# Kernel tuning notes

Measured on AMD Instinct MI355X. Metric: run time of the kernel, lower is better.

The kernel has to match this reference:

```python
import jax, jax.numpy as jnp
import numpy as np

N = 100_000
E = 1_000_000
D = 64
NORM_FACTOR = 100.0
LN_EPS = 1e-5


def setup_inputs() -> dict:
    key = jax.random.key(0)
    ks = jax.random.split(key, 8)
    h = jax.random.normal(ks[0], (N, D), dtype=jnp.float32)
    distances = jax.random.uniform(ks[1], (E, 1), dtype=jnp.float32)
    edges = jax.random.randint(ks[2], (2, E), 0, N, dtype=jnp.int64)
    node_mask = jnp.ones((N, 1), dtype=jnp.float32)
    edge_mask = jnp.ones((E, 1), dtype=jnp.float32)
    s = 1.0 / np.sqrt(D)
    W_lin = jax.random.normal(ks[3], (D, D), dtype=jnp.float32) * s
    b_lin = jnp.zeros((D,), dtype=jnp.float32)
    att_W1 = jax.random.normal(ks[4], (D, 2 * D + 1), dtype=jnp.float32) * (1.0 / np.sqrt(2 * D + 1))
    att_b1 = jnp.zeros((D,), dtype=jnp.float32)
    att_W2 = jax.random.normal(ks[5], (1, D), dtype=jnp.float32) * s
    att_b2 = jnp.zeros((1,), dtype=jnp.float32)
    ln_g = jnp.ones((D,), dtype=jnp.float32)
    ln_b = jnp.zeros((D,), dtype=jnp.float32)
    return {"h": h, "distances": distances, "edges": edges, "node_mask": node_mask,
            "edge_mask": edge_mask, "W_lin": W_lin, "b_lin": b_lin,
            "att_W1": att_W1, "att_b1": att_b1, "att_W2": att_W2, "att_b2": att_b2,
            "ln_g": ln_g, "ln_b": ln_b}


def reference(h, distances, edges, node_mask, edge_mask, W_lin, b_lin,
              att_W1, att_b1, att_W2, att_b2, ln_g, ln_b):
    # Linear projection: [N, D]
    x = h @ W_lin.T + b_lin
    row, col = edges[0], edges[1]
    x_row = x[row]          # [E, D]
    x_col = x[col]          # [E, D]
    # DenseAtt: MLP(concat(x_row, x_col, dist)) -> sigmoid -> * edge_mask
    cat = jnp.concatenate([x_row, x_col, distances], axis=1)  # [E, 2D+1]
    hdn = jax.nn.silu(cat @ att_W1.T + att_b1)                # [E, D]
    att = jax.nn.sigmoid(hdn @ att_W2.T + att_b2) * edge_mask # [E, 1]
    # Attention-weighted scatter-sum aggregation into row segments
    agg = x_col * att
    out = jax.ops.segment_sum(agg, row, num_segments=x.shape[0]) / NORM_FACTOR
    out = out + x           # residual
    # LayerNorm + activation
    mu = jnp.mean(out, axis=-1, keepdims=True)
    var = jnp.mean(jnp.square(out - mu), axis=-1, keepdims=True)
    y = (out - mu) * jax.lax.rsqrt(var + LN_EPS) * ln_g + ln_b
    return jax.nn.silu(y)
```

## Files before the change

kernel.cpp:

```cpp
#include <hip/hip_runtime.h>
#include <hip/hip_bf16.h>

#define N_NODES 100000
#define N_EDGES 1000000
#define DIM 64
#define NORM_INV 0.01f
#define LN_EPS 1e-5f
#define N_TILES 6250
#define PROJ_BLOCKS 1563
#define N_BUCKETS 782
#define NB_PAD 800
#define HISTB 489
#define SC_EDGES 4096
#define SC_BLOCKS 245
#define L2E 1.4426950408889634f
#define LN2 0.6931471805599453f
#define CAP 2560

typedef __attribute__((ext_vector_type(8))) short short8;
typedef __attribute__((ext_vector_type(4))) float f32x4;

__device__ __forceinline__ unsigned short f2bf(float f) {
    union { float f; unsigned u; } x; x.f = f;
    unsigned r = x.u + 0x7FFFu + ((x.u >> 16) & 1u);
    return (unsigned short)(r >> 16);
}
__device__ __forceinline__ float bf2f(unsigned short s) {
    union { unsigned u; float f; } x; x.u = ((unsigned)s) << 16; return x.f;
}

__global__ __launch_bounds__(256) void prep_frags(
    const float* __restrict__ W, const float* __restrict__ att_W1,
    const float* __restrict__ att_b1, const float* __restrict__ att_W2,
    short8* __restrict__ whi, short8* __restrict__ wlo,
    short8* __restrict__ wa, short8* __restrict__ wb,
    float4* __restrict__ tab) {
    const int l = threadIdx.x & 63;
    const int nt = threadIdx.x >> 6;
    const int c = l & 15, q = l >> 4;
    const int n = nt * 16 + c;
#pragma unroll
    for (int ks = 0; ks < 2; ++ks) {
        const int k0 = ks * 32 + q * 8;
        short8 hi8, lo8, a8, b8;
#pragma unroll
        for (int jj = 0; jj < 8; ++jj) {
            float w = W[n * 64 + k0 + jj];
            unsigned short hh = f2bf(w);
            hi8[jj] = (short)hh;
            lo8[jj] = (short)f2bf(w - bf2f(hh));
            a8[jj] = (short)f2bf(att_W1[n * 129 + k0 + jj]);
            b8[jj] = (short)f2bf(att_W1[n * 129 + 64 + k0 + jj]);
        }
        const int idx = (nt * 2 + ks) * 64 + l;
        whi[idx] = hi8; wlo[idx] = lo8; wa[idx] = a8; wb[idx] = b8;
    }
    if (threadIdx.x < 64) {
        const int f = threadIdx.x;
        tab[f] = make_float4(att_W2[f] * LN2, att_W1[f * 129 + 128] * L2E,
                             att_b1[f] * L2E, 0.f);
    }
}

__global__ __launch_bounds__(256) void proj_hist(
    const float* __restrict__ h, const float* __restrict__ bl,
    const short8* __restrict__ whi, const short8* __restrict__ wlo,
    const short8* __restrict__ wa, const short8* __restrict__ wb,
    const int* __restrict__ edges, int* __restrict__ bucketCnt,
    unsigned short* __restrict__ xv, unsigned short* __restrict__ u_bf) {
    if (blockIdx.x >= PROJ_BLOCKS) {
        __shared__ int lh[N_BUCKETS];
        const int tid = threadIdx.x;
        for (int i = tid; i < N_BUCKETS; i += 256) lh[i] = 0;
        __syncthreads();
        const int e0 = (blockIdx.x - PROJ_BLOCKS) * 2048;
#pragma unroll
        for (int i = 0; i < 8; ++i) {
            const int e = e0 + tid * 8 + i;
            if (e < N_EDGES) atomicAdd(&lh[edges[e] >> 7], 1);
        }
        __syncthreads();
        for (int b = tid; b < N_BUCKETS; b += 256)
            if (lh[b]) atomicAdd(&bucketCnt[b], lh[b]);
        return;
    }
    __shared__ __align__(16) unsigned short lds[4][16 * 72];
    const int lane = threadIdx.x & 63;
    const int wv = threadIdx.x >> 6;
    const int c = lane & 15, q = lane >> 4;
    const int tile = blockIdx.x * 4 + wv;
    if (tile >= N_TILES) return;
    const int n0 = tile * 16;

    short8 Whi[4][2], Wlo[4][2], Wa[4][2], Wb[4][2];
    float bias[4];
#pragma unroll
    for (int nt = 0; nt < 4; ++nt) {
        bias[nt] = bl[nt * 16 + c];
#pragma unroll
        for (int ks = 0; ks < 2; ++ks) {
            const int idx = (nt * 2 + ks) * 64 + lane;
            Whi[nt][ks] = whi[idx]; Wlo[nt][ks] = wlo[idx];
            Wa[nt][ks] = wa[idx];   Wb[nt][ks] = wb[idx];
        }
    }

    short8 Ahi[2], Alo[2];
#pragma unroll
    for (int ks = 0; ks < 2; ++ks) {
        const float* hp = h + (size_t)(n0 + c) * 64 + ks * 32 + q * 8;
        f32x4 p0 = *(const f32x4*)hp;
        f32x4 p1 = *(const f32x4*)(hp + 4);
        short8 hi8, lo8;
#pragma unroll
        for (int jj = 0; jj < 4; ++jj) {
            unsigned short hh = f2bf(p0[jj]);
            hi8[jj] = (short)hh; lo8[jj] = (short)f2bf(p0[jj] - bf2f(hh));
            unsigned short h2 = f2bf(p1[jj]);
            hi8[4 + jj] = (short)h2; lo8[4 + jj] = (short)f2bf(p1[jj] - bf2f(h2));
        }
        Ahi[ks] = hi8; Alo[ks] = lo8;
    }

    f32x4 xacc[4] = {{0,0,0,0},{0,0,0,0},{0,0,0,0},{0,0,0,0}};
#pragma unroll
    for (int ks = 0; ks < 2; ++ks)
#pragma unroll
        for (int nt = 0; nt < 4; ++nt) {
            xacc[nt] = __builtin_amdgcn_mfma_f32_16x16x32_bf16(Ahi[ks], Whi[nt][ks], xacc[nt], 0, 0, 0);
            xacc[nt] = __builtin_amdgcn_mfma_f32_16x16x32_bf16(Ahi[ks], Wlo[nt][ks], xacc[nt], 0, 0, 0);
            xacc[nt] = __builtin_amdgcn_mfma_f32_16x16x32_bf16(Alo[ks], Whi[nt][ks], xacc[nt], 0, 0, 0);
        }

    unsigned short* lw = lds[wv];
#pragma unroll
    for (int r = 0; r < 4; ++r) {
        const int node = n0 + q * 4 + r;
        unsigned short xb[4];
#pragma unroll
        for (int nt = 0; nt < 4; ++nt) {
            unsigned short v16 = f2bf(xacc[nt][r] + bias[nt]);
            xb[nt] = v16;
            lw[(q * 4 + r) * 72 + nt * 16 + c] = v16;
        }
        uint2 pk;
        pk.x = (unsigned)xb[0] | ((unsigned)xb[1] << 16);
        pk.y = (unsigned)xb[2] | ((unsigned)xb[3] << 16);
        *(uint2*)(xv + (size_t)node * 128 + c * 8) = pk;
    }

    short8 Ax[2];
#pragma unroll
    for (int ks = 0; ks < 2; ++ks)
        Ax[ks] = *(const short8*)&lw[c * 72 + ks * 32 + q * 8];

    f32x4 uacc[4] = {{0,0,0,0},{0,0,0,0},{0,0,0,0},{0,0,0,0}};
    f32x4 vacc[4] = {{0,0,0,0},{0,0,0,0},{0,0,0,0},{0,0,0,0}};
#pragma unroll
    for (int ks = 0; ks < 2; ++ks)
#pragma unroll
        for (int nt = 0; nt < 4; ++nt) {
            uacc[nt] = __builtin_amdgcn_mfma_f32_16x16x32_bf16(Ax[ks], Wa[nt][ks], uacc[nt], 0, 0, 0);
            vacc[nt] = __builtin_amdgcn_mfma_f32_16x16x32_bf16(Ax[ks], Wb[nt][ks], vacc[nt], 0, 0, 0);
        }
#pragma unroll
    for (int r = 0; r < 4; ++r) {
        const int node = n0 + q * 4 + r;
        uint2 pu;
        pu.x = (unsigned)f2bf(uacc[0][r] * L2E) | ((unsigned)f2bf(uacc[1][r] * L2E) << 16);
        pu.y = (unsigned)f2bf(uacc[2][r] * L2E) | ((unsigned)f2bf(uacc[3][r] * L2E) << 16);
        *(uint2*)(u_bf + (size_t)node * 64 + c * 4) = pu;
        uint2 pk;
        pk.x = (unsigned)f2bf(vacc[0][r] * L2E) | ((unsigned)f2bf(vacc[1][r] * L2E) << 16);
        pk.y = (unsigned)f2bf(vacc[2][r] * L2E) | ((unsigned)f2bf(vacc[3][r] * L2E) << 16);
        *(uint2*)(xv + (size_t)node * 128 + c * 8 + 4) = pk;
    }
}

__global__ __launch_bounds__(1024) void scanA(
    const int* __restrict__ bucketCnt, int* __restrict__ baseA,
    int* __restrict__ cursA) {
    __shared__ int wsum[16];
    const int t = threadIdx.x, lane = t & 63, w = t >> 6;
    const int v = (t < N_BUCKETS) ? bucketCnt[t] : 0;
    int sc = v;
#pragma unroll
    for (int off = 1; off < 64; off <<= 1) {
        int u = __shfl_up(sc, off);
        if (lane >= off) sc += u;
    }
    if (lane == 63) wsum[w] = sc;
    __syncthreads();
    if (w == 0) {
        int x = (lane < 16) ? wsum[lane] : 0;
#pragma unroll
        for (int off = 1; off < 16; off <<= 1) {
            int u = __shfl_up(x, off);
            if (lane >= off) x += u;
        }
        if (lane < 16) wsum[lane] = x;
    }
    __syncthreads();
    const int excl = sc - v + ((w > 0) ? wsum[w - 1] : 0);
    if (t < N_BUCKETS) { baseA[t] = excl; cursA[t] = excl; }
    if (t == N_BUCKETS - 1) baseA[N_BUCKETS] = excl + v;
}

__global__ __launch_bounds__(256) void scatterB(
    const int* __restrict__ edges, const float* __restrict__ dist,
    const float* __restrict__ emask, int* __restrict__ cursA,
    uint2* __restrict__ srec) {
    __shared__ int lh[NB_PAD];
    __shared__ int lofs[NB_PAD];
    __shared__ int lb[NB_PAD];
    __shared__ __align__(16) uint2 lsort[SC_EDGES];
    __shared__ unsigned short gb[SC_EDGES];
    __shared__ int wsum[4];

    const int tid = threadIdx.x;
    const int lane = tid & 63;
    const int w = tid >> 6;
    for (int i = tid; i < NB_PAD; i += 256) lh[i] = 0;
    __syncthreads();

    const int eb = blockIdx.x * SC_EDGES;
    const int total = min(SC_EDGES, N_EDGES - eb);

    int rows[16], rank[16];
    uint2 recs[16];
    const int e0 = eb + tid * 16;
#pragma unroll
    for (int g = 0; g < 4; ++g) {
        const int e = e0 + g * 4;
        if (e + 4 <= N_EDGES) {
            const int4 rr = *(const int4*)(edges + e);
            const int4 cc = *(const int4*)(edges + N_EDGES + e);
            const float4 dd = *(const float4*)(dist + e);
            const float4 mm = *(const float4*)(emask + e);
            rows[g*4+0] = rr.x; rows[g*4+1] = rr.y; rows[g*4+2] = rr.z; rows[g*4+3] = rr.w;
            const int c4[4] = {cc.x, cc.y, cc.z, cc.w};
            const float d4[4] = {dd.x, dd.y, dd.z, dd.w};
            const float m4[4] = {mm.x, mm.y, mm.z, mm.w};
#pragma unroll
            for (int i = 0; i < 4; ++i) {
                const int ii = g * 4 + i;
                recs[ii].x = (unsigned)c4[i] | ((unsigned)(rows[ii] & 127) << 24);
                recs[ii].y = (unsigned)f2bf(d4[i]) |
                             ((unsigned)f2bf(m4[i] * NORM_INV) << 16);
                rank[ii] = atomicAdd(&lh[rows[ii] >> 7], 1);
            }
        } else {
#pragma unroll
            for (int i = 0; i < 4; ++i) {
                const int ii = g * 4 + i;
                const int ee = e + i;
                if (ee < N_EDGES) {
                    rows[ii] = edges[ee];
                    recs[ii].x = (unsigned)edges[N_EDGES + ee] |
                                 ((unsigned)(rows[ii] & 127) << 24);
                    recs[ii].y = (unsigned)f2bf(dist[ee]) |
                                 ((unsigned)f2bf(emask[ee] * NORM_INV) << 16);
                    rank[ii] = atomicAdd(&lh[rows[ii] >> 7], 1);
                } else {
                    rows[ii] = -1;
                }
            }
        }
    }
    __syncthreads();

    const int b0 = tid * 4;
    int c0 = 0, c1 = 0, c2 = 0, c3 = 0;
    if (b0 < NB_PAD) { c0 = lh[b0]; c1 = lh[b0+1]; c2 = lh[b0+2]; c3 = lh[b0+3]; }
    const int S = c0 + c1 + c2 + c3;
    int sc = S;
#pragma unroll
    for (int off = 1; off < 64; off <<= 1) {
        int u = __shfl_up(sc, off);
        if (lane >= off) sc += u;
    }
    if (lane == 63) wsum[w] = sc;
    __syncthreads();
    int wbase = 0;
    if (w > 0) wbase = wsum[0];
    if (w > 1) wbase += wsum[1];
    if (w > 2) wbase += wsum[2];
    int excl = sc - S + wbase;
    if (b0 < N_BUCKETS) {
        lofs[b0] = excl;
        lofs[b0+1] = excl + c0;
        lofs[b0+2] = excl + c0 + c1;
        lofs[b0+3] = excl + c0 + c1 + c2;
        if (c0) lb[b0]   = atomicAdd(&cursA[b0],   c0);
        if (c1 && b0+1 < N_BUCKETS) lb[b0+1] = atomicAdd(&cursA[b0+1], c1);
        if (c2 && b0+2 < N_BUCKETS) lb[b0+2] = atomicAdd(&cursA[b0+2], c2);
        if (c3 && b0+3 < N_BUCKETS) lb[b0+3] = atomicAdd(&cursA[b0+3], c3);
    }
    __syncthreads();

#pragma unroll
    for (int i = 0; i < 16; ++i) {
        if (rows[i] >= 0) {
            const int bk = rows[i] >> 7;
            const int pos = lofs[bk] + rank[i];
            lsort[pos] = recs[i];
            gb[pos] = (unsigned short)bk;
        }
    }
    __syncthreads();

    for (int s = tid; s < total; s += 256) {
        const int bk = gb[s];
        const uint2 rc = lsort[s];
        srec[lb[bk] + (s - lofs[bk])] = rc;
    }
}

__global__ __launch_bounds__(512, 4) void agg_fused(
    const int* __restrict__ baseA, const uint2* __restrict__ srec,
    const unsigned short* __restrict__ xv, const unsigned short* __restrict__ u_bf,
    const float4* __restrict__ tab, const float* __restrict__ att_b2,
    const float* __restrict__ ln_g, const float* __restrict__ ln_b,
    float* __restrict__ out) {
    __shared__ __align__(16) uint2 lrecs[CAP + 16];
    __shared__ int hist[128];
    __shared__ int rst[129];
    __shared__ int cur[128];
    __shared__ int wtot;

    const int b = blockIdx.x;
    const int tid = threadIdx.x;
    const int lane = tid & 63;
    const int wv = tid >> 6;
    const int s0g = baseA[b];
    const int cnt = baseA[b + 1] - s0g;

    if (tid < 128) hist[tid] = 0;
    __syncthreads();

    uint2 rec0, rec1, rec2, rec3, rec4;
    int lr0 = -1, lr1 = -1, lr2 = -1, lr3 = -1, lr4 = -1;
    {
        int idx = tid;
        if (idx < cnt) { rec0 = srec[s0g + idx]; lr0 = (int)(rec0.x >> 24); rec0.x &= 0x00FFFFFFu; atomicAdd(&hist[lr0], 1); }
        idx += 512;
        if (idx < cnt) { rec1 = srec[s0g + idx]; lr1 = (int)(rec1.x >> 24); rec1.x &= 0x00FFFFFFu; atomicAdd(&hist[lr1], 1); }
        idx += 512;
        if (idx < cnt) { rec2 = srec[s0g + idx]; lr2 = (int)(rec2.x >> 24); rec2.x &= 0x00FFFFFFu; atomicAdd(&hist[lr2], 1); }
        idx += 512;
        if (idx < cnt) { rec3 = srec[s0g + idx]; lr3 = (int)(rec3.x >> 24); rec3.x &= 0x00FFFFFFu; atomicAdd(&hist[lr3], 1); }
        idx += 512;
        if (idx < cnt) { rec4 = srec[s0g + idx]; lr4 = (int)(rec4.x >> 24); rec4.x &= 0x00FFFFFFu; atomicAdd(&hist[lr4], 1); }
    }
    __syncthreads();

    int c = 0, p = 0, sc = 0;
    if (tid < 128) {
        c = hist[tid];
        p = (c + 3) & ~3;
        sc = p;
#pragma unroll
        for (int off = 1; off < 64; off <<= 1) {
            int u = __shfl_up(sc, off);
            if (lane >= off) sc += u;
        }
        if (tid == 63) wtot = sc;
    }
    __syncthreads();
    if (tid < 128) {
        if (tid >= 64) sc += wtot;
        const int excl = sc - p;
        rst[tid] = excl;
        cur[tid] = excl;
        uint2 z; z.x = 0; z.y = 0;
        for (int i = c; i < p; ++i) lrecs[excl + i] = z;
        if (tid == 127) {
            rst[128] = excl + p;
            for (int i = 0; i < 16; ++i) lrecs[excl + p + i] = z;
        }
    }
    __syncthreads();

    if (lr0 >= 0) lrecs[atomicAdd(&cur[lr0], 1)] = rec0;
    if (lr1 >= 0) lrecs[atomicAdd(&cur[lr1], 1)] = rec1;
    if (lr2 >= 0) lrecs[atomicAdd(&cur[lr2], 1)] = rec2;
    if (lr3 >= 0) lrecs[atomicAdd(&cur[lr3], 1)] = rec3;
    if (lr4 >= 0) lrecs[atomicAdd(&cur[lr4], 1)] = rec4;
    __syncthreads();

    const int j = lane & 15;
    const int sl = lane >> 4;
    const float4 t0 = tab[j], t1 = tab[j + 16], t2 = tab[j + 32], t3 = tab[j + 48];
    const float b2L = att_b2[0] * L2E;
    const float gg = ln_g[lane], bb = ln_b[lane];
    const unsigned* xvu = (const unsigned*)xv;

#pragma unroll 1
    for (int k = 0; k < 16; ++k) {
        const int lrw = wv + 8 * k;
        const int r = b * 128 + lrw;
        if (r >= N_NODES) break;

        const uint2 uu = *(const uint2*)(u_bf + (size_t)r * 64 + j * 4);
        const float base0 = __uint_as_float(uu.x << 16) + t0.z;
        const float base1 = __uint_as_float(uu.x & 0xffff0000u) + t1.z;
        const float base2 = __uint_as_float(uu.y << 16) + t2.z;
        const float base3 = __uint_as_float(uu.y & 0xffff0000u) + t3.z;

        const int s0 = rst[lrw];
        const int e1 = rst[lrw + 1];

        float a0 = 0.f, a1 = 0.f, a2 = 0.f, a3 = 0.f;
        if (e1 > s0) {
            uint2 recA = lrecs[s0 + sl];
            uint4 xvA = *(const uint4*)(xvu + (size_t)recA.x * 64 + j * 4);
            for (int e = s0; e < e1; e += 4) {
                const uint2 recB = lrecs[e + 4 + sl];
                const uint4 xvB = *(const uint4*)(xvu + (size_t)recB.x * 64 + j * 4);

                const float dist = __uint_as_float(recA.y << 16);
                const float emN = __uint_as_float(recA.y & 0xffff0000u);
                const float x0 = __uint_as_float(xvA.x << 16);
                const float x1 = __uint_as_float(xvA.x & 0xffff0000u);
                const float x2 = __uint_as_float(xvA.y << 16);
                const float x3 = __uint_as_float(xvA.y & 0xffff0000u);
                const float v0 = __uint_as_float(xvA.z << 16);
                const float v1 = __uint_as_float(xvA.z & 0xffff0000u);
                const float v2 = __uint_as_float(xvA.w << 16);
                const float v3 = __uint_as_float(xvA.w & 0xffff0000u);
                float pv = 0.f, pre, sg;
                pre = fmaf(dist, t0.y, base0) + v0;
                sg = __builtin_amdgcn_rcpf(1.f + __builtin_amdgcn_exp2f(-pre));
                pv = fmaf(pre * sg, t0.x, pv);
                pre = fmaf(dist, t1.y, base1) + v1;
                sg = __builtin_amdgcn_rcpf(1.f + __builtin_amdgcn_exp2f(-pre));
                pv = fmaf(pre * sg, t1.x, pv);
                pre = fmaf(dist, t2.y, base2) + v2;
                sg = __builtin_amdgcn_rcpf(1.f + __builtin_amdgcn_exp2f(-pre));
                pv = fmaf(pre * sg, t2.x, pv);
                pre = fmaf(dist, t3.y, base3) + v3;
                sg = __builtin_amdgcn_rcpf(1.f + __builtin_amdgcn_exp2f(-pre));
                pv = fmaf(pre * sg, t3.x, pv);
                pv += __shfl_xor(pv, 1); pv += __shfl_xor(pv, 2);
                pv += __shfl_xor(pv, 4); pv += __shfl_xor(pv, 8);
                const float sp = fmaf(pv, L2E, b2L);
                const float att =
                    emN * __builtin_amdgcn_rcpf(1.f + __builtin_amdgcn_exp2f(-sp));
                a0 = fmaf(att, x0, a0); a1 = fmaf(att, x1, a1);
                a2 = fmaf(att, x2, a2); a3 = fmaf(att, x3, a3);
                recA = recB; xvA = xvB;
            }
        }
        a0 += __shfl_xor(a0, 16); a0 += __shfl_xor(a0, 32);
        a1 += __shfl_xor(a1, 16); a1 += __shfl_xor(a1, 32);
        a2 += __shfl_xor(a2, 16); a2 += __shfl_xor(a2, 32);
        a3 += __shfl_xor(a3, 16); a3 += __shfl_xor(a3, 32);

        const uint2 xr = *(const uint2*)(xvu + (size_t)r * 64 + j * 4);
        const float o0 = __uint_as_float(xr.x << 16) + a0;
        const float o1 = __uint_as_float(xr.x & 0xffff0000u) + a1;
        const float o2 = __uint_as_float(xr.y << 16) + a2;
        const float o3 = __uint_as_float(xr.y & 0xffff0000u) + a3;

        float ssum = o0 + o1 + o2 + o3;
        ssum += __shfl_xor(ssum, 1); ssum += __shfl_xor(ssum, 2);
        ssum += __shfl_xor(ssum, 4); ssum += __shfl_xor(ssum, 8);
        const float mu = ssum * (1.f / 64.f);
        const float d0 = o0 - mu, d1 = o1 - mu, d2 = o2 - mu, d3 = o3 - mu;
        float vs = d0 * d0 + d1 * d1 + d2 * d2 + d3 * d3;
        vs += __shfl_xor(vs, 1); vs += __shfl_xor(vs, 2);
        vs += __shfl_xor(vs, 4); vs += __shfl_xor(vs, 8);
        const float rstd = rsqrtf(vs * (1.f / 64.f) + LN_EPS);

        const float dk = (sl == 0) ? d0 : (sl == 1) ? d1 : (sl == 2) ? d2 : d3;
        const float y = fmaf(dk * rstd, gg, bb);
        out[(size_t)r * 64 + lane] =
            y * __builtin_amdgcn_rcpf(1.f + __builtin_amdgcn_exp2f(-y * L2E));
    }
}

extern "C" void kernel_launch(void* const* d_in, const int* in_sizes, int n_in,
                              void* d_out, int out_size, void* d_ws, size_t ws_size,
                              hipStream_t stream) {
    const float* h      = (const float*)d_in[0];
    const float* dist   = (const float*)d_in[1];
    const int*   edges  = (const int*)d_in[2];
    const float* emask  = (const float*)d_in[4];
    const float* W_lin  = (const float*)d_in[5];
    const float* b_lin  = (const float*)d_in[6];
    const float* att_W1 = (const float*)d_in[7];
    const float* att_b1 = (const float*)d_in[8];
    const float* att_W2 = (const float*)d_in[9];
    const float* att_b2 = (const float*)d_in[10];
    const float* ln_g   = (const float*)d_in[11];
    const float* ln_b   = (const float*)d_in[12];
    float* out = (float*)d_out;

    char* ws = (char*)d_ws;
    unsigned short* xv   = (unsigned short*)ws;
    unsigned short* u_bf = (unsigned short*)(ws + 25600000);
    uint2* srec          = (uint2*)(ws + 38400000);
    int* bucketCnt       = (int*)(ws + 46400000);
    int* baseA           = (int*)(ws + 46403200);
    int* cursA           = (int*)(ws + 46406400);
    float4* tab          = (float4*)(ws + 46409600);
    short8* whi          = (short8*)(ws + 46410624);
    short8* wlo          = (short8*)(ws + 46418816);
    short8* wa           = (short8*)(ws + 46427008);
    short8* wb           = (short8*)(ws + 46435200);

    hipMemsetAsync(bucketCnt, 0, N_BUCKETS * sizeof(int), stream);
    prep_frags<<<1, 256, 0, stream>>>(W_lin, att_W1, att_b1, att_W2,
                                      whi, wlo, wa, wb, tab);
    proj_hist<<<PROJ_BLOCKS + HISTB, 256, 0, stream>>>(
        h, b_lin, whi, wlo, wa, wb, edges, bucketCnt, xv, u_bf);
    scanA<<<1, 1024, 0, stream>>>(bucketCnt, baseA, cursA);
    scatterB<<<SC_BLOCKS, 256, 0, stream>>>(edges, dist, emask, cursA, srec);
    agg_fused<<<N_BUCKETS, 512, 0, stream>>>(baseA, srec, xv, u_bf,
                                             tab, att_b2, ln_g, ln_b, out);
}
```

Baseline: 232.9 us.

## Fuse edge bucketing into projection kernel and drop global scan pass

The edge histogram, global scan and scatter kernels are replaced by a per-block local bucket sort that runs inside the projection kernel. Each block writes its locally sorted edge chunk plus a per-block offset table, and the aggregation kernel gathers its bucket's records from all 245 chunks using that table. This removes a memset, two kernel launches, global atomics and the serial scan dependency. In exchange, agg_fused now reads with only 245 threads each walking a short strided range serially, and it does two passes over global records, which may cut memory-level parallelism there. The projection kernel's shared memory grows to a 39 KB pool, which may lower occupancy for the projection blocks.

```diff
diff --git a/kernel.cpp b/kernel.cpp
--- a/kernel.cpp
+++ b/kernel.cpp
@@ -10,9 +10,9 @@
 #define PROJ_BLOCKS 1563
 #define N_BUCKETS 782
 #define NB_PAD 800
-#define HISTB 489
 #define SC_EDGES 4096
 #define SC_BLOCKS 245
+#define OFS_STRIDE 784
 #define L2E 1.4426950408889634f
 #define LN2 0.6931471805599453f
 #define CAP 2560
@@ -62,29 +62,115 @@
     }
 }
 
-__global__ __launch_bounds__(256) void proj_hist(
+__global__ __launch_bounds__(256) void proj_scatter(
     const float* __restrict__ h, const float* __restrict__ bl,
     const short8* __restrict__ whi, const short8* __restrict__ wlo,
     const short8* __restrict__ wa, const short8* __restrict__ wb,
-    const int* __restrict__ edges, int* __restrict__ bucketCnt,
+    const int* __restrict__ edges, const float* __restrict__ dist,
+    const float* __restrict__ emask,
+    uint2* __restrict__ srec, int* __restrict__ ofsT,
     unsigned short* __restrict__ xv, unsigned short* __restrict__ u_bf) {
+    __shared__ __align__(16) char pool[39168];
+    __shared__ int wsum[4];
+
     if (blockIdx.x >= PROJ_BLOCKS) {
-        __shared__ int lh[N_BUCKETS];
+        int* lh = (int*)pool;
+        int* lofs = (int*)pool + NB_PAD;
+        uint2* lsort = (uint2*)(pool + 6400);
+        const int blk = blockIdx.x - PROJ_BLOCKS;
         const int tid = threadIdx.x;
-        for (int i = tid; i < N_BUCKETS; i += 256) lh[i] = 0;
+        const int lane = tid & 63;
+        const int w = tid >> 6;
+        for (int i = tid; i < NB_PAD; i += 256) lh[i] = 0;
         __syncthreads();
-        const int e0 = (blockIdx.x - PROJ_BLOCKS) * 2048;
-#pragma unroll
-        for (int i = 0; i < 8; ++i) {
-            const int e = e0 + tid * 8 + i;
-            if (e < N_EDGES) atomicAdd(&lh[edges[e] >> 7], 1);
+
+        const int eb = blk * SC_EDGES;
+        const int total = min(SC_EDGES, N_EDGES - eb);
+
+        int rows[16], rank[16];
+        uint2 recs[16];
+        const int e0 = eb + tid * 16;
+#pragma unroll
+        for (int g = 0; g < 4; ++g) {
+            const int e = e0 + g * 4;
+            if (e + 4 <= N_EDGES) {
+                const int4 rr = *(const int4*)(edges + e);
+                const int4 cc = *(const int4*)(edges + N_EDGES + e);
+                const float4 dd = *(const float4*)(dist + e);
+                const float4 mm = *(const float4*)(emask + e);
+                rows[g*4+0] = rr.x; rows[g*4+1] = rr.y; rows[g*4+2] = rr.z; rows[g*4+3] = rr.w;
+                const int c4[4] = {cc.x, cc.y, cc.z, cc.w};
+                const float d4[4] = {dd.x, dd.y, dd.z, dd.w};
+                const float m4[4] = {mm.x, mm.y, mm.z, mm.w};
+#pragma unroll
+                for (int i = 0; i < 4; ++i) {
+                    const int ii = g * 4 + i;
+                    recs[ii].x = (unsigned)c4[i] | ((unsigned)(rows[ii] & 127) << 24);
+                    recs[ii].y = (unsigned)f2bf(d4[i]) |
+                                 ((unsigned)f2bf(m4[i] * NORM_INV) << 16);
+                    rank[ii] = atomicAdd(&lh[rows[ii] >> 7], 1);
+                }
+            } else {
+#pragma unroll
+                for (int i = 0; i < 4; ++i) {
+                    const int ii = g * 4 + i;
+                    const int ee = e + i;
+                    if (ee < N_EDGES) {
+                        rows[ii] = edges[ee];
+                        recs[ii].x = (unsigned)edges[N_EDGES + ee] |
+                                     ((unsigned)(rows[ii] & 127) << 24);
+                        recs[ii].y = (unsigned)f2bf(dist[ee]) |
+                                     ((unsigned)f2bf(emask[ee] * NORM_INV) << 16);
+                        rank[ii] = atomicAdd(&lh[rows[ii] >> 7], 1);
+                    } else {
+                        rows[ii] = -1;
+                    }
+                }
+            }
         }
         __syncthreads();
-        for (int b = tid; b < N_BUCKETS; b += 256)
-            if (lh[b]) atomicAdd(&bucketCnt[b], lh[b]);
+
+        const int b0 = tid * 4;
+        int c0 = 0, c1 = 0, c2 = 0, c3 = 0;
+        if (b0 < NB_PAD) { c0 = lh[b0]; c1 = lh[b0+1]; c2 = lh[b0+2]; c3 = lh[b0+3]; }
+        const int S = c0 + c1 + c2 + c3;
+        int sc = S;
+#pragma unroll
+        for (int off = 1; off < 64; off <<= 1) {
+            int u = __shfl_up(sc, off);
+            if (lane >= off) sc += u;
+        }
+        if (lane == 63) wsum[w] = sc;
+        __syncthreads();
+        int wbase = 0;
+        if (w > 0) wbase = wsum[0];
+        if (w > 1) wbase += wsum[1];
+        if (w > 2) wbase += wsum[2];
+        const int excl = sc - S + wbase;
+        if (b0 < NB_PAD) {
+            lofs[b0] = excl;
+            lofs[b0+1] = excl + c0;
+            lofs[b0+2] = excl + c0 + c1;
+            lofs[b0+3] = excl + c0 + c1 + c2;
+        }
+        __syncthreads();
+
+#pragma unroll
+        for (int i = 0; i < 16; ++i) {
+            if (rows[i] >= 0) {
+                const int bk = rows[i] >> 7;
+                lsort[lofs[bk] + rank[i]] = recs[i];
+            }
+        }
+        __syncthreads();
+
+        for (int s = tid; s < total; s += 256)
+            srec[(size_t)blk * SC_EDGES + s] = lsort[s];
+        for (int b = tid; b < 783; b += 256)
+            ofsT[blk * OFS_STRIDE + b] = lofs[b];
         return;
     }
-    __shared__ __align__(16) unsigned short lds[4][16 * 72];
+
     const int lane = threadIdx.x & 63;
     const int wv = threadIdx.x >> 6;
     const int c = lane & 15, q = lane >> 4;
@@ -132,7 +218,7 @@
             xacc[nt] = __builtin_amdgcn_mfma_f32_16x16x32_bf16(Alo[ks], Whi[nt][ks], xacc[nt], 0, 0, 0);
         }
 
-    unsigned short* lw = lds[wv];
+    unsigned short* lw = (unsigned short*)pool + wv * (16 * 72);
 #pragma unroll
     for (int r = 0; r < 4; ++r) {
         const int node = n0 + q * 4 + r;
@@ -177,147 +263,8 @@
     }
 }
 
-__global__ __launch_bounds__(1024) void scanA(
-    const int* __restrict__ bucketCnt, int* __restrict__ baseA,
-    int* __restrict__ cursA) {
-    __shared__ int wsum[16];
-    const int t = threadIdx.x, lane = t & 63, w = t >> 6;
-    const int v = (t < N_BUCKETS) ? bucketCnt[t] : 0;
-    int sc = v;
-#pragma unroll
-    for (int off = 1; off < 64; off <<= 1) {
-        int u = __shfl_up(sc, off);
-        if (lane >= off) sc += u;
-    }
-    if (lane == 63) wsum[w] = sc;
-    __syncthreads();
-    if (w == 0) {
-        int x = (lane < 16) ? wsum[lane] : 0;
-#pragma unroll
-        for (int off = 1; off < 16; off <<= 1) {
-            int u = __shfl_up(x, off);
-            if (lane >= off) x += u;
-        }
-        if (lane < 16) wsum[lane] = x;
-    }
-    __syncthreads();
-    const int excl = sc - v + ((w > 0) ? wsum[w - 1] : 0);
-    if (t < N_BUCKETS) { baseA[t] = excl; cursA[t] = excl; }
-    if (t == N_BUCKETS - 1) baseA[N_BUCKETS] = excl + v;
-}
-
-__global__ __launch_bounds__(256) void scatterB(
-    const int* __restrict__ edges, const float* __restrict__ dist,
-    const float* __restrict__ emask, int* __restrict__ cursA,
-    uint2* __restrict__ srec) {
-    __shared__ int lh[NB_PAD];
-    __shared__ int lofs[NB_PAD];
-    __shared__ int lb[NB_PAD];
-    __shared__ __align__(16) uint2 lsort[SC_EDGES];
-    __shared__ unsigned short gb[SC_EDGES];
-    __shared__ int wsum[4];
-
-    const int tid = threadIdx.x;
-    const int lane = tid & 63;
-    const int w = tid >> 6;
-    for (int i = tid; i < NB_PAD; i += 256) lh[i] = 0;
-    __syncthreads();
-
-    const int eb = blockIdx.x * SC_EDGES;
-    const int total = min(SC_EDGES, N_EDGES - eb);
-
-    int rows[16], rank[16];
-    uint2 recs[16];
-    const int e0 = eb + tid * 16;
-#pragma unroll
-    for (int g = 0; g < 4; ++g) {
-        const int e = e0 + g * 4;
-        if (e + 4 <= N_EDGES) {
-            const int4 rr = *(const int4*)(edges + e);
-            const int4 cc = *(const int4*)(edges + N_EDGES + e);
-            const float4 dd = *(const float4*)(dist + e);
-            const float4 mm = *(const float4*)(emask + e);
-            rows[g*4+0] = rr.x; rows[g*4+1] = rr.y; rows[g*4+2] = rr.z; rows[g*4+3] = rr.w;
-            const int c4[4] = {cc.x, cc.y, cc.z, cc.w};
-            const float d4[4] = {dd.x, dd.y, dd.z, dd.w};
-            const float m4[4] = {mm.x, mm.y, mm.z, mm.w};
-#pragma unroll
-            for (int i = 0; i < 4; ++i) {
-                const int ii = g * 4 + i;
-                recs[ii].x = (unsigned)c4[i] | ((unsigned)(rows[ii] & 127) << 24);
-                recs[ii].y = (unsigned)f2bf(d4[i]) |
-                             ((unsigned)f2bf(m4[i] * NORM_INV) << 16);
-                rank[ii] = atomicAdd(&lh[rows[ii] >> 7], 1);
-            }
-        } else {
-#pragma unroll
-            for (int i = 0; i < 4; ++i) {
-                const int ii = g * 4 + i;
-                const int ee = e + i;
-                if (ee < N_EDGES) {
-                    rows[ii] = edges[ee];
-                    recs[ii].x = (unsigned)edges[N_EDGES + ee] |
-                                 ((unsigned)(rows[ii] & 127) << 24);
-                    recs[ii].y = (unsigned)f2bf(dist[ee]) |
-                                 ((unsigned)f2bf(emask[ee] * NORM_INV) << 16);
-                    rank[ii] = atomicAdd(&lh[rows[ii] >> 7], 1);
-                } else {
-                    rows[ii] = -1;
-                }
-            }
-        }
-    }
-    __syncthreads();
-
-    const int b0 = tid * 4;
-    int c0 = 0, c1 = 0, c2 = 0, c3 = 0;
-    if (b0 < NB_PAD) { c0 = lh[b0]; c1 = lh[b0+1]; c2 = lh[b0+2]; c3 = lh[b0+3]; }
-    const int S = c0 + c1 + c2 + c3;
-    int sc = S;
-#pragma unroll
-    for (int off = 1; off < 64; off <<= 1) {
-        int u = __shfl_up(sc, off);
-        if (lane >= off) sc += u;
-    }
-    if (lane == 63) wsum[w] = sc;
-    __syncthreads();
-    int wbase = 0;
-    if (w > 0) wbase = wsum[0];
-    if (w > 1) wbase += wsum[1];
-    if (w > 2) wbase += wsum[2];
-    int excl = sc - S + wbase;
-    if (b0 < N_BUCKETS) {
-        lofs[b0] = excl;
-        lofs[b0+1] = excl + c0;
-        lofs[b0+2] = excl + c0 + c1;
-        lofs[b0+3] = excl + c0 + c1 + c2;
-        if (c0) lb[b0]   = atomicAdd(&cursA[b0],   c0);
-        if (c1 && b0+1 < N_BUCKETS) lb[b0+1] = atomicAdd(&cursA[b0+1], c1);
-        if (c2 && b0+2 < N_BUCKETS) lb[b0+2] = atomicAdd(&cursA[b0+2], c2);
-        if (c3 && b0+3 < N_BUCKETS) lb[b0+3] = atomicAdd(&cursA[b0+3], c3);
-    }
-    __syncthreads();
-
-#pragma unroll
-    for (int i = 0; i < 16; ++i) {
-        if (rows[i] >= 0) {
-            const int bk = rows[i] >> 7;
-            const int pos = lofs[bk] + rank[i];
-            lsort[pos] = recs[i];
-            gb[pos] = (unsigned short)bk;
-        }
-    }
-    __syncthreads();
-
-    for (int s = tid; s < total; s += 256) {
-        const int bk = gb[s];
-        const uint2 rc = lsort[s];
-        srec[lb[bk] + (s - lofs[bk])] = rc;
-    }
-}
-
 __global__ __launch_bounds__(512, 4) void agg_fused(
-    const int* __restrict__ baseA, const uint2* __restrict__ srec,
+    const uint2* __restrict__ srec, const int* __restrict__ ofsT,
     const unsigned short* __restrict__ xv, const unsigned short* __restrict__ u_bf,
     const float4* __restrict__ tab, const float* __restrict__ att_b2,
     const float* __restrict__ ln_g, const float* __restrict__ ln_b,
@@ -332,25 +279,18 @@
     const int tid = threadIdx.x;
     const int lane = tid & 63;
     const int wv = tid >> 6;
-    const int s0g = baseA[b];
-    const int cnt = baseA[b + 1] - s0g;
 
     if (tid < 128) hist[tid] = 0;
     __syncthreads();
 
-    uint2 rec0, rec1, rec2, rec3, rec4;
-    int lr0 = -1, lr1 = -1, lr2 = -1, lr3 = -1, lr4 = -1;
-    {
-        int idx = tid;
-        if (idx < cnt) { rec0 = srec[s0g + idx]; lr0 = (int)(rec0.x >> 24); rec0.x &= 0x00FFFFFFu; atomicAdd(&hist[lr0], 1); }
-        idx += 512;
-        if (idx < cnt) { rec1 = srec[s0g + idx]; lr1 = (int)(rec1.x >> 24); rec1.x &= 0x00FFFFFFu; atomicAdd(&hist[lr1], 1); }
-        idx += 512;
-        if (idx < cnt) { rec2 = srec[s0g + idx]; lr2 = (int)(rec2.x >> 24); rec2.x &= 0x00FFFFFFu; atomicAdd(&hist[lr2], 1); }
-        idx += 512;
-        if (idx < cnt) { rec3 = srec[s0g + idx]; lr3 = (int)(rec3.x >> 24); rec3.x &= 0x00FFFFFFu; atomicAdd(&hist[lr3], 1); }
-        idx += 512;
-        if (idx < cnt) { rec4 = srec[s0g + idx]; lr4 = (int)(rec4.x >> 24); rec4.x &= 0x00FFFFFFu; atomicAdd(&hist[lr4], 1); }
+    int st = 0, en = 0;
+    if (tid < SC_BLOCKS) {
+        st = ofsT[tid * OFS_STRIDE + b];
+        en = ofsT[tid * OFS_STRIDE + b + 1];
+        const unsigned* sx = (const unsigned*)srec;
+        const size_t gb = (size_t)tid * SC_EDGES;
+        for (int i = st; i < en; ++i)
+            atomicAdd(&hist[sx[2 * (gb + i)] >> 24], 1);
     }
     __syncthreads();
 
@@ -381,11 +321,15 @@
     }
     __syncthreads();
 
-    if (lr0 >= 0) lrecs[atomicAdd(&cur[lr0], 1)] = rec0;
-    if (lr1 >= 0) lrecs[atomicAdd(&cur[lr1], 1)] = rec1;
-    if (lr2 >= 0) lrecs[atomicAdd(&cur[lr2], 1)] = rec2;
-    if (lr3 >= 0) lrecs[atomicAdd(&cur[lr3], 1)] = rec3;
-    if (lr4 >= 0) lrecs[atomicAdd(&cur[lr4], 1)] = rec4;
+    if (tid < SC_BLOCKS) {
+        const size_t gb = (size_t)tid * SC_EDGES;
+        for (int i = st; i < en; ++i) {
+            uint2 rec = srec[gb + i];
+            const int lr = (int)(rec.x >> 24);
+            rec.x &= 0x00FFFFFFu;
+            lrecs[atomicAdd(&cur[lr], 1)] = rec;
+        }
+    }
     __syncthreads();
 
     const int j = lane & 15;
@@ -500,22 +444,17 @@
     unsigned short* xv   = (unsigned short*)ws;
     unsigned short* u_bf = (unsigned short*)(ws + 25600000);
     uint2* srec          = (uint2*)(ws + 38400000);
-    int* bucketCnt       = (int*)(ws + 46400000);
-    int* baseA           = (int*)(ws + 46403200);
-    int* cursA           = (int*)(ws + 46406400);
-    float4* tab          = (float4*)(ws + 46409600);
-    short8* whi          = (short8*)(ws + 46410624);
-    short8* wlo          = (short8*)(ws + 46418816);
-    short8* wa           = (short8*)(ws + 46427008);
-    short8* wb           = (short8*)(ws + 46435200);
-
-    hipMemsetAsync(bucketCnt, 0, N_BUCKETS * sizeof(int), stream);
+    int* ofsT            = (int*)(ws + 46428160);
+    float4* tab          = (float4*)(ws + 47196480);
+    short8* whi          = (short8*)(ws + 47197504);
+    short8* wlo          = (short8*)(ws + 47205696);
+    short8* wa           = (short8*)(ws + 47213888);
+    short8* wb           = (short8*)(ws + 47222080);
+
     prep_frags<<<1, 256, 0, stream>>>(W_lin, att_W1, att_b1, att_W2,
                                       whi, wlo, wa, wb, tab);
-    proj_hist<<<PROJ_BLOCKS + HISTB, 256, 0, stream>>>(
-        h, b_lin, whi, wlo, wa, wb, edges, bucketCnt, xv, u_bf);
-    scanA<<<1, 1024, 0, stream>>>(bucketCnt, baseA, cursA);
-    scatterB<<<SC_BLOCKS, 256, 0, stream>>>(edges, dist, emask, cursA, srec);
-    agg_fused<<<N_BUCKETS, 512, 0, stream>>>(baseA, srec, xv, u_bf,
+    proj_scatter<<<PROJ_BLOCKS + SC_BLOCKS, 256, 0, stream>>>(
+        h, b_lin, whi, wlo, wa, wb, edges, dist, emask, srec, ofsT, xv, u_bf);
+    agg_fused<<<N_BUCKETS, 512, 0, stream>>>(srec, ofsT, xv, u_bf,
                                              tab, att_b2, ln_g, ln_b, out);
 }
```

Measured after the change: 211.5 us. -9.2%, faster.
